# Optimization experiments

Hardware: AMD Instinct MI355X
Metric: run time of the kernel (lower is better)

Reference implementation:

```python
import jax, jax.numpy as jnp
import numpy as np
from jax import lax

B, T, I, H, O = 256, 128, 512, 1024, 512


def setup_inputs() -> dict:
    key = jax.random.key(0)
    ks = jax.random.split(key, 7)
    s = 1.0 / np.sqrt(H)  # PyTorch LSTM/Linear init bound
    x = jax.random.normal(ks[0], (B, T, I), dtype=jnp.float32)
    W_ih = jax.random.uniform(ks[1], (4 * H, I), jnp.float32, -s, s)
    W_hh = jax.random.uniform(ks[2], (4 * H, H), jnp.float32, -s, s)
    b_ih = jax.random.uniform(ks[3], (4 * H,), jnp.float32, -s, s)
    b_hh = jax.random.uniform(ks[4], (4 * H,), jnp.float32, -s, s)
    W_fc = jax.random.uniform(ks[5], (O, H), jnp.float32, -s, s)
    b_fc = jax.random.uniform(ks[6], (O,), jnp.float32, -s, s)
    return {"x": x, "W_ih": W_ih, "W_hh": W_hh, "b_ih": b_ih,
            "b_hh": b_hh, "W_fc": W_fc, "b_fc": b_fc}


def _lstm_last(x, W_ih, W_hh, b_ih, b_hh):
    # Precompute input contribution for all timesteps: [T, B, 4H]
    pre = jnp.einsum('bti,gi->tbg', x, W_ih) + b_ih + b_hh

    def step(carry, xg):
        h, c = carry
        gates = xg + h @ W_hh.T  # [B, 4H]
        i, f, g, o = jnp.split(gates, 4, axis=-1)  # PyTorch gate order i,f,g,o
        c = jax.nn.sigmoid(f) * c + jax.nn.sigmoid(i) * jnp.tanh(g)
        h = jax.nn.sigmoid(o) * jnp.tanh(c)
        return (h, c), None

    h0 = jnp.zeros((x.shape[0], W_hh.shape[1]), x.dtype)
    (h, c), _ = lax.scan(step, (h0, h0), pre)
    return h, c


def reference(x, W_ih, W_hh, b_ih, b_hh, W_fc, b_fc):
    h, c = _lstm_last(x, W_ih, W_hh, b_ih, b_hh)
    out = h @ W_fc.T + b_fc  # fc on last timestep hidden
    # hidden returned as (h_n, c_n) with leading n_layers=1 dim, as in PyTorch
    return out, (h[None], c[None])
```

## Files before the change

kernel.cpp:

```cpp
#include <hip/hip_runtime.h>

typedef short bf8 __attribute__((ext_vector_type(8)));
typedef float f32x4 __attribute__((ext_vector_type(4)));
typedef uint u32x4 __attribute__((ext_vector_type(4)));

static constexpr int BB = 256;
static constexpr int TT = 128;
static constexpr int II = 512;
static constexpr int HH = 1024;
static constexpr int OO = 512;
static constexpr int G4 = 4096;

static constexpr size_t OUT_H = (size_t)BB * OO;
static constexpr size_t OUT_C = OUT_H + (size_t)BB * HH;
static constexpr size_t HBUF  = (size_t)BB * HH;

__device__ __forceinline__ float bf2f(ushort u) {
    unsigned v = ((unsigned)u) << 16;
    return __builtin_bit_cast(float, v);
}
__device__ __forceinline__ ushort f2bf(float f) {
    unsigned x = __builtin_bit_cast(unsigned, f);
    x = x + 0x7FFFu + ((x >> 16) & 1u);
    return (ushort)(x >> 16);
}
__device__ __forceinline__ float sigf(float x) { return 1.0f / (1.0f + __expf(-x)); }
__device__ __forceinline__ float tanhf_(float x) { return 2.0f * sigf(2.0f * x) - 1.0f; }

__device__ __forceinline__ void st_wt_short(const ushort* p, uint v) {
    asm volatile("global_store_short %0, %1, off sc0 sc1" :: "v"(p), "v"(v) : "memory");
}
__device__ __forceinline__ void st_wt_b64(const ushort* p, uint2 v) {
    asm volatile("global_store_dwordx2 %0, %1, off sc0 sc1" :: "v"(p), "v"(v) : "memory");
}
__device__ __forceinline__ void ld_bp_ushort_issue(uint& dst, const ushort* p) {
    asm volatile("global_load_ushort %0, %1, off sc0 sc1" : "=v"(dst) : "v"(p) : "memory");
}
__device__ __forceinline__ void ld_bp_b128_issue(u32x4& dst, const ushort* p) {
    asm volatile("global_load_dwordx4 %0, %1, off sc0 sc1" : "=v"(dst) : "v"(p) : "memory");
}
__device__ __forceinline__ void wait_vm0() {
    asm volatile("s_waitcnt vmcnt(0)" ::: "memory");
    __builtin_amdgcn_sched_barrier(0);
}
#define WAITVM(N) do { asm volatile("s_waitcnt vmcnt(" #N ")" ::: "memory"); \
                       __builtin_amdgcn_sched_barrier(0); } while (0)

__device__ __forceinline__ void poll_all64(const int* base, int thr) {
    int l = threadIdx.x & 63;
    const int* p = base + (l << 5);
    int v;
    for (;;) {
        asm volatile("global_load_dword %0, %1, off sc0 sc1\n\ts_waitcnt vmcnt(0)"
                     : "=v"(v) : "v"(p) : "memory");
        if (__all(v >= thr)) break;
        __builtin_amdgcn_s_sleep(1);
    }
    __builtin_amdgcn_sched_barrier(0);
}
__device__ __forceinline__ void flag_store(int* slot, int v) {
    asm volatile("global_store_dword %0, %1, off sc0 sc1" :: "v"(slot), "v"(v) : "memory");
}

__global__ void k_init(int* flags) {
    int i = blockIdx.x * 256 + threadIdx.x;
    if (i < 16384) flags[i] = 0;
}

__global__ void k_cast(const float* __restrict__ src, ushort* __restrict__ dst, int n4) {
    int i = blockIdx.x * blockDim.x + threadIdx.x;
    int stride = gridDim.x * blockDim.x;
    for (; i < n4; i += stride) {
        float4 v = ((const float4*)src)[i];
        ushort4 o;
        o.x = f2bf(v.x); o.y = f2bf(v.y); o.z = f2bf(v.z); o.w = f2bf(v.w);
        ((ushort4*)dst)[i] = o;
    }
}

__global__ void k_prep_w(const float* __restrict__ w, ushort* __restrict__ wp,
                         const float* __restrict__ bi, const float* __restrict__ bh,
                         float* __restrict__ bp, int Kdim) {
    int p = blockIdx.x;
    int orig = ((p >> 4) & 3) * HH + ((p >> 6) << 4) + (p & 15);
    const float* src = w + (size_t)orig * Kdim;
    ushort* dst = wp + (size_t)p * Kdim;
    for (int k = threadIdx.x; k < Kdim; k += 256) dst[k] = f2bf(src[k]);
    if (threadIdx.x == 0 && bp) bp[p] = bi[orig] + bh[orig];
}

__global__ __launch_bounds__(256) void k_main(
    const float* __restrict__ x, const ushort* __restrict__ wpih,
    const float* __restrict__ bp, ushort* __restrict__ pre,
    const ushort* __restrict__ wphh, ushort* __restrict__ hbf,
    float* __restrict__ dout, int* flags, int SEG) {
    __shared__ ushort wl[32 * 2048];
    __shared__ ushort Al[64 * 32];
    __shared__ ushort Bl[128 * 32];

    int tid = threadIdx.x;
    int bid = blockIdx.x;
    int g = (bid >> 1) & 3;
    int j = ((bid & 1) << 5) | (bid >> 3);
    int row0 = g << 6;
    int* stepf = flags + g * 2048;
    int* segf  = flags + 8192 + g * 2048;
    int* mystep = stepf + j * 32;
    int* myseg  = segf + j * 32;
    int nseg = TT / SEG;

    int w = tid >> 6, l = tid & 63;
    int l15 = l & 15, kg = l >> 4;
    int wbase = ((l15 << 6) + (kg << 4)) ^ ((l15 & 7) << 4);

    {
        const ushort* wsrc = wphh + (size_t)(j << 6) * HH;
        for (int s = 0; s < 32; ++s) {
            int cidx = (s << 8) + tid;
            int c = cidx >> 7;
            int kc = cidx & 127;
            uint4 v = *(const uint4*)(wsrc + (size_t)c * HH + (kc << 3));
            int byte = ((kc >> 2) << 12) + ((((c << 6) + ((kc & 3) << 4))) ^ ((c & 7) << 4));
            *(uint4*)((char*)wl + byte) = v;
        }
        int r = tid >> 2, hc = (tid & 3) << 2;
        uint2 z; z.x = 0; z.y = 0;
        st_wt_b64(hbf + (size_t)(row0 + r) * HH + (j << 4) + hc, z);
    }
    wait_vm0();
    __syncthreads();
    if (tid == 0) flag_store(mystep, 1);

    int wm = w >> 1, wn = w & 1;
    int r0 = tid >> 2, kk = tid & 3;
    int sbyteA = ((r0 << 6) + (kk << 4)) ^ ((r0 & 7) << 4);
    int sbyteB1 = sbyteA + 4096;

    const ushort* hbase = hbf + (size_t)(row0 + (w << 4) + l15) * HH + (kg << 3);
    int drow = row0 + (w << 4) + (kg << 2);
    int hcol = (j << 4) + l15;
    ushort* hobase = hbf + (size_t)drow * HH + hcol;
    const ushort* pbase = pre + (size_t)drow * G4 + (j << 6) + l15;
    float creg[4] = {0.f, 0.f, 0.f, 0.f};

    for (int sg = 0; sg < nseg; ++sg) {
        int t0 = sg * SEG;
        if (sg > 0) poll_all64(stepf, t0 + 1);

        int ntiles = SEG << 5;
        for (int q = j; q < ntiles; q += 64) {
            int trel = q >> 5;
            int t = t0 + trel;
            int n0 = (q & 31) << 7;
            const float* xa = x + ((size_t)(row0 + r0) * TT + t) * II + (kk << 3);
            const ushort* gb0 = wpih + (size_t)(n0 + r0) * II + (kk << 3);
            const ushort* gb1 = gb0 + (size_t)64 * II;
            f32x4 acc[2][4];
#pragma unroll
            for (int mi = 0; mi < 2; ++mi)
#pragma unroll
                for (int ni = 0; ni < 4; ++ni) acc[mi][ni] = f32x4{0.f, 0.f, 0.f, 0.f};
            float4 a0 = *(const float4*)xa;
            float4 a1 = *(const float4*)(xa + 4);
            uint4 b0v = *(const uint4*)gb0;
            uint4 b1v = *(const uint4*)gb1;
            for (int ko = 0; ko < 16; ++ko) {
                union { ushort us[8]; uint4 v; } pa;
                pa.us[0] = f2bf(a0.x); pa.us[1] = f2bf(a0.y); pa.us[2] = f2bf(a0.z); pa.us[3] = f2bf(a0.w);
                pa.us[4] = f2bf(a1.x); pa.us[5] = f2bf(a1.y); pa.us[6] = f2bf(a1.z); pa.us[7] = f2bf(a1.w);
                __syncthreads();
                *(uint4*)((char*)Al + sbyteA) = pa.v;
                *(uint4*)((char*)Bl + sbyteA) = b0v;
                *(uint4*)((char*)Bl + sbyteB1) = b1v;
                __syncthreads();
                if (ko < 15) {
                    int k = (ko + 1) << 5;
                    a0 = *(const float4*)(xa + k);
                    a1 = *(const float4*)(xa + k + 4);
                    b0v = *(const uint4*)(gb0 + k);
                    b1v = *(const uint4*)(gb1 + k);
                }
                bf8 af[2], bv[4];
#pragma unroll
                for (int mi = 0; mi < 2; ++mi)
                    af[mi] = *(const bf8*)((char*)Al + wm * 2048 + mi * 1024 + wbase);
#pragma unroll
                for (int ni = 0; ni < 4; ++ni)
                    bv[ni] = *(const bf8*)((char*)Bl + wn * 4096 + ni * 1024 + wbase);
#pragma unroll
                for (int mi = 0; mi < 2; ++mi)
#pragma unroll
                    for (int ni = 0; ni < 4; ++ni)
                        acc[mi][ni] = __builtin_amdgcn_mfma_f32_16x16x32_bf16(af[mi], bv[ni], acc[mi][ni], 0, 0, 0);
            }
#pragma unroll
            for (int ni = 0; ni < 4; ++ni) {
                int col = n0 + wn * 64 + ni * 16 + l15;
                float bias = bp[col];
#pragma unroll
                for (int mi = 0; mi < 2; ++mi) {
                    int arow = row0 + wm * 32 + mi * 16 + (kg << 2);
#pragma unroll
                    for (int r = 0; r < 4; ++r)
                        st_wt_short(pre + ((size_t)trel * BB + arow + r) * G4 + col,
                                    (uint)f2bf(acc[mi][ni][r] + bias));
                }
            }
        }
        wait_vm0();
        __syncthreads();
        if (tid == 0) flag_store(myseg, sg + 1);
        poll_all64(segf, sg + 1);

        uint prn[16];
#pragma unroll
        for (int ni = 0; ni < 4; ++ni)
#pragma unroll
            for (int r = 0; r < 4; ++r)
                ld_bp_ushort_issue(prn[ni * 4 + r], pbase + (size_t)r * G4 + (ni << 4));
        wait_vm0();

        for (int trel = 0; trel < SEG; ++trel) {
            int t = t0 + trel;
            poll_all64(stepf, t + 1);
            const ushort* hr = hbase + (size_t)(t & 1) * HBUF;
            u32x4 xv[8], yv[8];

#define ISSUE8(B, C) \
            _Pragma("unroll") \
            for (int u = 0; u < 8; ++u) ld_bp_b128_issue(B[u], hr + (((C) * 8 + u) << 5));
#define CONSUME8(B, C) \
            _Pragma("unroll") \
            for (int u = 0; u < 8; ++u) { \
                int ko = (C) * 8 + u; \
                bf8 a = __builtin_bit_cast(bf8, B[u]); \
                _Pragma("unroll") \
                for (int ni = 0; ni < 4; ++ni) { \
                    bf8 b = *(const bf8*)((char*)wl + ko * 4096 + ni * 1024 + wbase); \
                    acc[ni] = __builtin_amdgcn_mfma_f32_16x16x32_bf16(a, b, acc[ni], 0, 0, 0); \
                } \
            }

            f32x4 acc[4];
            ISSUE8(xv, 0)
            ISSUE8(yv, 1)
#pragma unroll
            for (int ni = 0; ni < 4; ++ni)
#pragma unroll
                for (int r = 0; r < 4; ++r) acc[ni][r] = bf2f((ushort)prn[ni * 4 + r]);
            WAITVM(8);
            CONSUME8(xv, 0)
            ISSUE8(xv, 2)
            WAITVM(8);
            CONSUME8(yv, 1)
            ISSUE8(yv, 3)
            WAITVM(8);
            CONSUME8(xv, 2)
            {
                int nrel = (trel + 1 < SEG) ? trel + 1 : 0;
                const ushort* pnn = pre + ((size_t)nrel * BB + drow) * G4 + (j << 6) + l15;
#pragma unroll
                for (int ni = 0; ni < 4; ++ni)
#pragma unroll
                    for (int r = 0; r < 4; ++r)
                        ld_bp_ushort_issue(prn[ni * 4 + r], pnn + (size_t)r * G4 + (ni << 4));
            }
            WAITVM(16);
            CONSUME8(yv, 3)
#undef ISSUE8
#undef CONSUME8

            ushort* ho = hobase + (size_t)((t & 1) ^ 1) * HBUF;
            bool last = (t == TT - 1);
#pragma unroll
            for (int r = 0; r < 4; ++r) {
                float ig = sigf(acc[0][r]);
                float fg = sigf(acc[1][r]);
                float gg = tanhf_(acc[2][r]);
                float og = sigf(acc[3][r]);
                float c = fg * creg[r] + ig * gg;
                creg[r] = c;
                float h = og * tanhf_(c);
                st_wt_short(ho + (size_t)r * HH, (uint)f2bf(h));
                if (last) {
                    dout[OUT_H + (size_t)(drow + r) * HH + hcol] = h;
                    dout[OUT_C + (size_t)(drow + r) * HH + hcol] = c;
                }
            }
            wait_vm0();
            __syncthreads();
            if (tid == 0) flag_store(mystep, t + 2);
        }
    }
}

__global__ __launch_bounds__(256) void k_fc(const ushort* __restrict__ hlast,
                                            const ushort* __restrict__ wfc,
                                            const float* __restrict__ bfc,
                                            float* __restrict__ out) {
    int tid = threadIdx.x;
    int b0 = (blockIdx.x >> 3) << 6;
    int n0 = (blockIdx.x & 7) << 6;
    int w = tid >> 6, l = tid & 63;
    int l15 = l & 15, kg = l >> 4;
    const ushort* ha = hlast + (size_t)(b0 + (w << 4) + l15) * HH + (kg << 3);
    f32x4 acc[4];
#pragma unroll
    for (int ni = 0; ni < 4; ++ni) acc[ni] = f32x4{0.f, 0.f, 0.f, 0.f};
    for (int ko = 0; ko < 32; ++ko) {
        bf8 a = *(const bf8*)(ha + (ko << 5));
#pragma unroll
        for (int ni = 0; ni < 4; ++ni) {
            bf8 b = *(const bf8*)(wfc + (size_t)(n0 + ni * 16 + l15) * HH + (ko << 5) + (kg << 3));
            acc[ni] = __builtin_amdgcn_mfma_f32_16x16x32_bf16(a, b, acc[ni], 0, 0, 0);
        }
    }
    int drow = b0 + (w << 4) + (kg << 2);
#pragma unroll
    for (int ni = 0; ni < 4; ++ni) {
        int col = n0 + ni * 16 + l15;
        float bias = bfc[col];
#pragma unroll
        for (int r = 0; r < 4; ++r)
            out[(size_t)(drow + r) * OO + col] = acc[ni][r] + bias;
    }
}

extern "C" void kernel_launch(void* const* d_in, const int* in_sizes, int n_in,
                              void* d_out, int out_size, void* d_ws, size_t ws_size,
                              hipStream_t stream) {
    const float* x   = (const float*)d_in[0];
    const float* Wih = (const float*)d_in[1];
    const float* Whh = (const float*)d_in[2];
    const float* bih = (const float*)d_in[3];
    const float* bhh = (const float*)d_in[4];
    const float* Wfc = (const float*)d_in[5];
    const float* bfc = (const float*)d_in[6];
    float* out = (float*)d_out;

    char* ws = (char*)d_ws;
    size_t off = 0;
    ushort* wpih = (ushort*)(ws + off); off += (size_t)G4 * II * 2;
    ushort* wphh = (ushort*)(ws + off); off += (size_t)G4 * HH * 2;
    ushort* wfcb = (ushort*)(ws + off); off += (size_t)OO * HH * 2;
    float*  bp   = (float*)(ws + off);  off += (size_t)G4 * 4;
    int*    flags= (int*)(ws + off);    off += 16384 * 4;
    ushort* hbf  = (ushort*)(ws + off); off += (size_t)2 * BB * HH * 2;
    size_t fixed = off;
    int SEG = 16;
    while (SEG > 1 && fixed + (size_t)SEG * BB * G4 * 2 > ws_size) SEG >>= 1;
    ushort* pre = (ushort*)(ws + fixed);

    k_init<<<64, 256, 0, stream>>>(flags);
    k_cast<<<256, 256, 0, stream>>>(Wfc, wfcb, OO * HH / 4);
    k_prep_w<<<G4, 256, 0, stream>>>(Wih, wpih, bih, bhh, bp, II);
    k_prep_w<<<G4, 256, 0, stream>>>(Whh, wphh, nullptr, nullptr, nullptr, HH);
    k_main<<<256, 256, 0, stream>>>(x, wpih, bp, pre, wphh, hbf, out, flags, SEG);
    k_fc<<<32, 256, 0, stream>>>(hbf, wfcb, bfc, out);
}
```

Baseline: 1.705 ms.

## Interleave input-projection tiles with recurrent steps using double-buffered pre segments

The input projection for the next segment is now computed between recurrent steps, writing into a second pre buffer. This replaces the previous pattern of a full projection phase followed by a segment-wide barrier. The goal is to fill the idle time that each block spends waiting on per-step flags, and to drop the extra segment synchronization. The change also stages pre-activation tiles and h outputs through LDS so they can be written with 128-bit stores instead of scattered short stores, and it remaps blocks so that the 64 blocks of a batch group are contiguous. The costs are a larger pre buffer (two segments), extra LDS, and tileA work sitting on the per-step critical path, which may lengthen each step's latency.

```diff
diff --git a/kernel.cpp b/kernel.cpp
--- a/kernel.cpp
+++ b/kernel.cpp
@@ -27,11 +27,11 @@
 __device__ __forceinline__ float sigf(float x) { return 1.0f / (1.0f + __expf(-x)); }
 __device__ __forceinline__ float tanhf_(float x) { return 2.0f * sigf(2.0f * x) - 1.0f; }
 
-__device__ __forceinline__ void st_wt_short(const ushort* p, uint v) {
-    asm volatile("global_store_short %0, %1, off sc0 sc1" :: "v"(p), "v"(v) : "memory");
-}
 __device__ __forceinline__ void st_wt_b64(const ushort* p, uint2 v) {
     asm volatile("global_store_dwordx2 %0, %1, off sc0 sc1" :: "v"(p), "v"(v) : "memory");
+}
+__device__ __forceinline__ void st_wt_b128(const ushort* p, u32x4 v) {
+    asm volatile("global_store_dwordx4 %0, %1, off sc0 sc1" :: "v"(p), "v"(v) : "memory");
 }
 __device__ __forceinline__ void ld_bp_ushort_issue(uint& dst, const ushort* p) {
     asm volatile("global_load_ushort %0, %1, off sc0 sc1" : "=v"(dst) : "v"(p) : "memory");
@@ -64,7 +64,7 @@
 
 __global__ void k_init(int* flags) {
     int i = blockIdx.x * 256 + threadIdx.x;
-    if (i < 16384) flags[i] = 0;
+    if (i < 8192) flags[i] = 0;
 }
 
 __global__ void k_cast(const float* __restrict__ src, ushort* __restrict__ dst, int n4) {
@@ -89,6 +89,78 @@
     if (threadIdx.x == 0 && bp) bp[p] = bi[orig] + bh[orig];
 }
 
+__device__ __forceinline__ void tileA(
+    const float* __restrict__ x, const ushort* __restrict__ wpih,
+    const float* __restrict__ bp, ushort* __restrict__ dst,
+    int t, int trel_out, int n0, int row0,
+    ushort* Al, ushort* Bl, ushort* packT,
+    int tid, int wm, int wn, int r0, int kk,
+    int sbyteA, int sbyteB1, int wbase, int l15, int kg) {
+    const float* xa = x + ((size_t)(row0 + r0) * TT + t) * II + (kk << 3);
+    const ushort* gb0 = wpih + (size_t)(n0 + r0) * II + (kk << 3);
+    const ushort* gb1 = gb0 + (size_t)64 * II;
+    f32x4 acc[2][4];
+#pragma unroll
+    for (int mi = 0; mi < 2; ++mi)
+#pragma unroll
+        for (int ni = 0; ni < 4; ++ni) acc[mi][ni] = f32x4{0.f, 0.f, 0.f, 0.f};
+    float4 a0 = *(const float4*)xa;
+    float4 a1 = *(const float4*)(xa + 4);
+    uint4 b0v = *(const uint4*)gb0;
+    uint4 b1v = *(const uint4*)gb1;
+    for (int ko = 0; ko < 16; ++ko) {
+        union { ushort us[8]; uint4 v; } pa;
+        pa.us[0] = f2bf(a0.x); pa.us[1] = f2bf(a0.y); pa.us[2] = f2bf(a0.z); pa.us[3] = f2bf(a0.w);
+        pa.us[4] = f2bf(a1.x); pa.us[5] = f2bf(a1.y); pa.us[6] = f2bf(a1.z); pa.us[7] = f2bf(a1.w);
+        __syncthreads();
+        *(uint4*)((char*)Al + sbyteA) = pa.v;
+        *(uint4*)((char*)Bl + sbyteA) = b0v;
+        *(uint4*)((char*)Bl + sbyteB1) = b1v;
+        __syncthreads();
+        if (ko < 15) {
+            int k = (ko + 1) << 5;
+            a0 = *(const float4*)(xa + k);
+            a1 = *(const float4*)(xa + k + 4);
+            b0v = *(const uint4*)(gb0 + k);
+            b1v = *(const uint4*)(gb1 + k);
+        }
+        bf8 af[2], bv[4];
+#pragma unroll
+        for (int mi = 0; mi < 2; ++mi)
+            af[mi] = *(const bf8*)((char*)Al + wm * 2048 + mi * 1024 + wbase);
+#pragma unroll
+        for (int ni = 0; ni < 4; ++ni)
+            bv[ni] = *(const bf8*)((char*)Bl + wn * 4096 + ni * 1024 + wbase);
+#pragma unroll
+        for (int mi = 0; mi < 2; ++mi)
+#pragma unroll
+            for (int ni = 0; ni < 4; ++ni)
+                acc[mi][ni] = __builtin_amdgcn_mfma_f32_16x16x32_bf16(af[mi], bv[ni], acc[mi][ni], 0, 0, 0);
+    }
+#pragma unroll
+    for (int ni = 0; ni < 4; ++ni) {
+        int col = wn * 64 + ni * 16 + l15;
+        float bias = bp[n0 + col];
+#pragma unroll
+        for (int mi = 0; mi < 2; ++mi) {
+            int rloc = wm * 32 + mi * 16 + (kg << 2);
+#pragma unroll
+            for (int r = 0; r < 4; ++r)
+                packT[(rloc + r) * 128 + col] = f2bf(acc[mi][ni][r] + bias);
+        }
+    }
+    __syncthreads();
+    const ushort* base = dst + ((size_t)trel_out * BB + row0) * G4 + n0;
+#pragma unroll
+    for (int s = 0; s < 4; ++s) {
+        int cidx = (s << 8) + tid;
+        int rloc = cidx >> 4;
+        int cc = (cidx & 15) << 3;
+        u32x4 v = *(const u32x4*)(packT + rloc * 128 + cc);
+        st_wt_b128(base + (size_t)rloc * G4 + cc, v);
+    }
+}
+
 __global__ __launch_bounds__(256) void k_main(
     const float* __restrict__ x, const ushort* __restrict__ wpih,
     const float* __restrict__ bp, ushort* __restrict__ pre,
@@ -97,17 +169,16 @@
     __shared__ ushort wl[32 * 2048];
     __shared__ ushort Al[64 * 32];
     __shared__ ushort Bl[128 * 32];
+    __shared__ ushort packT[64 * 128];
 
     int tid = threadIdx.x;
     int bid = blockIdx.x;
-    int g = (bid >> 1) & 3;
-    int j = ((bid & 1) << 5) | (bid >> 3);
+    int g = bid >> 6, j = bid & 63;
     int row0 = g << 6;
     int* stepf = flags + g * 2048;
-    int* segf  = flags + 8192 + g * 2048;
     int* mystep = stepf + j * 32;
-    int* myseg  = segf + j * 32;
     int nseg = TT / SEG;
+    size_t SEGEL = (size_t)SEG * BB * G4;
 
     int w = tid >> 6, l = tid & 63;
     int l15 = l & 15, kg = l >> 4;
@@ -127,9 +198,6 @@
         uint2 z; z.x = 0; z.y = 0;
         st_wt_b64(hbf + (size_t)(row0 + r) * HH + (j << 4) + hc, z);
     }
-    wait_vm0();
-    __syncthreads();
-    if (tid == 0) flag_store(mystep, 1);
 
     int wm = w >> 1, wn = w & 1;
     int r0 = tid >> 2, kk = tid & 3;
@@ -139,158 +207,114 @@
     const ushort* hbase = hbf + (size_t)(row0 + (w << 4) + l15) * HH + (kg << 3);
     int drow = row0 + (w << 4) + (kg << 2);
     int hcol = (j << 4) + l15;
-    ushort* hobase = hbf + (size_t)drow * HH + hcol;
-    const ushort* pbase = pre + (size_t)drow * G4 + (j << 6) + l15;
     float creg[4] = {0.f, 0.f, 0.f, 0.f};
 
-    for (int sg = 0; sg < nseg; ++sg) {
-        int t0 = sg * SEG;
-        if (sg > 0) poll_all64(stepf, t0 + 1);
-
-        int ntiles = SEG << 5;
-        for (int q = j; q < ntiles; q += 64) {
-            int trel = q >> 5;
-            int t = t0 + trel;
-            int n0 = (q & 31) << 7;
-            const float* xa = x + ((size_t)(row0 + r0) * TT + t) * II + (kk << 3);
-            const ushort* gb0 = wpih + (size_t)(n0 + r0) * II + (kk << 3);
-            const ushort* gb1 = gb0 + (size_t)64 * II;
-            f32x4 acc[2][4];
-#pragma unroll
-            for (int mi = 0; mi < 2; ++mi)
-#pragma unroll
-                for (int ni = 0; ni < 4; ++ni) acc[mi][ni] = f32x4{0.f, 0.f, 0.f, 0.f};
-            float4 a0 = *(const float4*)xa;
-            float4 a1 = *(const float4*)(xa + 4);
-            uint4 b0v = *(const uint4*)gb0;
-            uint4 b1v = *(const uint4*)gb1;
-            for (int ko = 0; ko < 16; ++ko) {
-                union { ushort us[8]; uint4 v; } pa;
-                pa.us[0] = f2bf(a0.x); pa.us[1] = f2bf(a0.y); pa.us[2] = f2bf(a0.z); pa.us[3] = f2bf(a0.w);
-                pa.us[4] = f2bf(a1.x); pa.us[5] = f2bf(a1.y); pa.us[6] = f2bf(a1.z); pa.us[7] = f2bf(a1.w);
-                __syncthreads();
-                *(uint4*)((char*)Al + sbyteA) = pa.v;
-                *(uint4*)((char*)Bl + sbyteA) = b0v;
-                *(uint4*)((char*)Bl + sbyteB1) = b1v;
-                __syncthreads();
-                if (ko < 15) {
-                    int k = (ko + 1) << 5;
-                    a0 = *(const float4*)(xa + k);
-                    a1 = *(const float4*)(xa + k + 4);
-                    b0v = *(const uint4*)(gb0 + k);
-                    b1v = *(const uint4*)(gb1 + k);
-                }
-                bf8 af[2], bv[4];
-#pragma unroll
-                for (int mi = 0; mi < 2; ++mi)
-                    af[mi] = *(const bf8*)((char*)Al + wm * 2048 + mi * 1024 + wbase);
-#pragma unroll
-                for (int ni = 0; ni < 4; ++ni)
-                    bv[ni] = *(const bf8*)((char*)Bl + wn * 4096 + ni * 1024 + wbase);
-#pragma unroll
-                for (int mi = 0; mi < 2; ++mi)
-#pragma unroll
-                    for (int ni = 0; ni < 4; ++ni)
-                        acc[mi][ni] = __builtin_amdgcn_mfma_f32_16x16x32_bf16(af[mi], bv[ni], acc[mi][ni], 0, 0, 0);
+    for (int q = j; q < SEG * 32; q += 64)
+        tileA(x, wpih, bp, pre, q >> 5, q >> 5, (q & 31) << 7, row0,
+              Al, Bl, packT, tid, wm, wn, r0, kk, sbyteA, sbyteB1, wbase, l15, kg);
+    wait_vm0();
+    __syncthreads();
+    if (tid == 0) flag_store(mystep, 1);
+    poll_all64(stepf, 1);
+
+    uint prn[16];
+    for (int t = 0; t < TT; ++t) {
+        int sg = t / SEG;
+        int trel = t - sg * SEG;
+        const ushort* sb = pre + (size_t)(sg & 1) * SEGEL;
+
+        if (trel == 0) {
+            const ushort* pb = sb + (size_t)drow * G4 + (j << 6) + l15;
+#pragma unroll
+            for (int ni = 0; ni < 4; ++ni)
+#pragma unroll
+                for (int r = 0; r < 4; ++r)
+                    ld_bp_ushort_issue(prn[ni * 4 + r], pb + (size_t)r * G4 + (ni << 4));
+            wait_vm0();
+        }
+
+        const ushort* hr = hbase + (size_t)(t & 1) * HBUF;
+        u32x4 xv[8], yv[8];
+#define ISSUE8(B, C) \
+        _Pragma("unroll") \
+        for (int u = 0; u < 8; ++u) ld_bp_b128_issue(B[u], hr + (((C) * 8 + u) << 5));
+#define CONSUME8(B, C) \
+        _Pragma("unroll") \
+        for (int u = 0; u < 8; ++u) { \
+            int ko = (C) * 8 + u; \
+            bf8 a = __builtin_bit_cast(bf8, B[u]); \
+            _Pragma("unroll") \
+            for (int ni = 0; ni < 4; ++ni) { \
+                bf8 b = *(const bf8*)((char*)wl + ko * 4096 + ni * 1024 + wbase); \
+                acc[ni] = __builtin_amdgcn_mfma_f32_16x16x32_bf16(a, b, acc[ni], 0, 0, 0); \
+            } \
+        }
+        f32x4 acc[4];
+        ISSUE8(xv, 0)
+        ISSUE8(yv, 1)
+#pragma unroll
+        for (int ni = 0; ni < 4; ++ni)
+#pragma unroll
+            for (int r = 0; r < 4; ++r) acc[ni][r] = bf2f((ushort)prn[ni * 4 + r]);
+        WAITVM(8);
+        CONSUME8(xv, 0)
+        ISSUE8(xv, 2)
+        WAITVM(8);
+        CONSUME8(yv, 1)
+        ISSUE8(yv, 3)
+        WAITVM(8);
+        CONSUME8(xv, 2)
+        if (trel < SEG - 1) {
+            const ushort* pnn = sb + ((size_t)(trel + 1) * BB + drow) * G4 + (j << 6) + l15;
+#pragma unroll
+            for (int ni = 0; ni < 4; ++ni)
+#pragma unroll
+                for (int r = 0; r < 4; ++r)
+                    ld_bp_ushort_issue(prn[ni * 4 + r], pnn + (size_t)r * G4 + (ni << 4));
+            WAITVM(16);
+        } else {
+            WAITVM(0);
+        }
+        CONSUME8(yv, 3)
+#undef ISSUE8
+#undef CONSUME8
+
+        bool last = (t == TT - 1);
+#pragma unroll
+        for (int r = 0; r < 4; ++r) {
+            float ig = sigf(acc[0][r]);
+            float fg = sigf(acc[1][r]);
+            float gg = tanhf_(acc[2][r]);
+            float og = sigf(acc[3][r]);
+            float c = fg * creg[r] + ig * gg;
+            creg[r] = c;
+            float h = og * tanhf_(c);
+            Al[((w << 4) + (kg << 2) + r) * 16 + l15] = f2bf(h);
+            if (last) {
+                dout[OUT_H + (size_t)(drow + r) * HH + hcol] = h;
+                dout[OUT_C + (size_t)(drow + r) * HH + hcol] = c;
             }
-#pragma unroll
-            for (int ni = 0; ni < 4; ++ni) {
-                int col = n0 + wn * 64 + ni * 16 + l15;
-                float bias = bp[col];
-#pragma unroll
-                for (int mi = 0; mi < 2; ++mi) {
-                    int arow = row0 + wm * 32 + mi * 16 + (kg << 2);
-#pragma unroll
-                    for (int r = 0; r < 4; ++r)
-                        st_wt_short(pre + ((size_t)trel * BB + arow + r) * G4 + col,
-                                    (uint)f2bf(acc[mi][ni][r] + bias));
-                }
-            }
+        }
+        __syncthreads();
+        if (tid < 128) {
+            u32x4 v = *(const u32x4*)(Al + (tid << 3));
+            const ushort* hop = hbf + (size_t)((t & 1) ^ 1) * HBUF
+                                + (size_t)(row0 + (tid >> 1)) * HH + (j << 4) + ((tid & 1) << 3);
+            st_wt_b128(hop, v);
         }
         wait_vm0();
         __syncthreads();
-        if (tid == 0) flag_store(myseg, sg + 1);
-        poll_all64(segf, sg + 1);
-
-        uint prn[16];
-#pragma unroll
-        for (int ni = 0; ni < 4; ++ni)
-#pragma unroll
-            for (int r = 0; r < 4; ++r)
-                ld_bp_ushort_issue(prn[ni * 4 + r], pbase + (size_t)r * G4 + (ni << 4));
-        wait_vm0();
-
-        for (int trel = 0; trel < SEG; ++trel) {
-            int t = t0 + trel;
-            poll_all64(stepf, t + 1);
-            const ushort* hr = hbase + (size_t)(t & 1) * HBUF;
-            u32x4 xv[8], yv[8];
-
-#define ISSUE8(B, C) \
-            _Pragma("unroll") \
-            for (int u = 0; u < 8; ++u) ld_bp_b128_issue(B[u], hr + (((C) * 8 + u) << 5));
-#define CONSUME8(B, C) \
-            _Pragma("unroll") \
-            for (int u = 0; u < 8; ++u) { \
-                int ko = (C) * 8 + u; \
-                bf8 a = __builtin_bit_cast(bf8, B[u]); \
-                _Pragma("unroll") \
-                for (int ni = 0; ni < 4; ++ni) { \
-                    bf8 b = *(const bf8*)((char*)wl + ko * 4096 + ni * 1024 + wbase); \
-                    acc[ni] = __builtin_amdgcn_mfma_f32_16x16x32_bf16(a, b, acc[ni], 0, 0, 0); \
-                } \
-            }
-
-            f32x4 acc[4];
-            ISSUE8(xv, 0)
-            ISSUE8(yv, 1)
-#pragma unroll
-            for (int ni = 0; ni < 4; ++ni)
-#pragma unroll
-                for (int r = 0; r < 4; ++r) acc[ni][r] = bf2f((ushort)prn[ni * 4 + r]);
-            WAITVM(8);
-            CONSUME8(xv, 0)
-            ISSUE8(xv, 2)
-            WAITVM(8);
-            CONSUME8(yv, 1)
-            ISSUE8(yv, 3)
-            WAITVM(8);
-            CONSUME8(xv, 2)
-            {
-                int nrel = (trel + 1 < SEG) ? trel + 1 : 0;
-                const ushort* pnn = pre + ((size_t)nrel * BB + drow) * G4 + (j << 6) + l15;
-#pragma unroll
-                for (int ni = 0; ni < 4; ++ni)
-#pragma unroll
-                    for (int r = 0; r < 4; ++r)
-                        ld_bp_ushort_issue(prn[ni * 4 + r], pnn + (size_t)r * G4 + (ni << 4));
-            }
-            WAITVM(16);
-            CONSUME8(yv, 3)
-#undef ISSUE8
-#undef CONSUME8
-
-            ushort* ho = hobase + (size_t)((t & 1) ^ 1) * HBUF;
-            bool last = (t == TT - 1);
-#pragma unroll
-            for (int r = 0; r < 4; ++r) {
-                float ig = sigf(acc[0][r]);
-                float fg = sigf(acc[1][r]);
-                float gg = tanhf_(acc[2][r]);
-                float og = sigf(acc[3][r]);
-                float c = fg * creg[r] + ig * gg;
-                creg[r] = c;
-                float h = og * tanhf_(c);
-                st_wt_short(ho + (size_t)r * HH, (uint)f2bf(h));
-                if (last) {
-                    dout[OUT_H + (size_t)(drow + r) * HH + hcol] = h;
-                    dout[OUT_C + (size_t)(drow + r) * HH + hcol] = c;
-                }
-            }
-            wait_vm0();
-            __syncthreads();
-            if (tid == 0) flag_store(mystep, t + 2);
-        }
+        if (tid == 0) flag_store(mystep, t + 2);
+
+        if ((trel & 1) == 0 && sg + 1 < nseg) {
+            int ti = trel >> 1;
+            int q = ti * 64 + j;
+            ushort* pn = pre + (size_t)((sg + 1) & 1) * SEGEL;
+            tileA(x, wpih, bp, pn, (sg + 1) * SEG + (q >> 5), q >> 5, (q & 31) << 7, row0,
+                  Al, Bl, packT, tid, wm, wn, r0, kk, sbyteA, sbyteB1, wbase, l15, kg);
+        }
+
+        if (t < TT - 1) poll_all64(stepf, t + 2);
     }
 }
 
@@ -344,14 +368,14 @@
     ushort* wphh = (ushort*)(ws + off); off += (size_t)G4 * HH * 2;
     ushort* wfcb = (ushort*)(ws + off); off += (size_t)OO * HH * 2;
     float*  bp   = (float*)(ws + off);  off += (size_t)G4 * 4;
-    int*    flags= (int*)(ws + off);    off += 16384 * 4;
+    int*    flags= (int*)(ws + off);    off += 8192 * 4;
     ushort* hbf  = (ushort*)(ws + off); off += (size_t)2 * BB * HH * 2;
     size_t fixed = off;
-    int SEG = 16;
-    while (SEG > 1 && fixed + (size_t)SEG * BB * G4 * 2 > ws_size) SEG >>= 1;
+    int SEG = 8;
+    while (SEG > 2 && fixed + (size_t)2 * SEG * BB * G4 * 2 > ws_size) SEG >>= 1;
     ushort* pre = (ushort*)(ws + fixed);
 
-    k_init<<<64, 256, 0, stream>>>(flags);
+    k_init<<<32, 256, 0, stream>>>(flags);
     k_cast<<<256, 256, 0, stream>>>(Wfc, wfcb, OO * HH / 4);
     k_prep_w<<<G4, 256, 0, stream>>>(Wih, wpih, bih, bhh, bp, II);
     k_prep_w<<<G4, 256, 0, stream>>>(Whh, wphh, nullptr, nullptr, nullptr, HH);
```

Result: faster. 1.583 ms (-7.2%).
